# Kernel optimization log

Hardware: AMD Instinct MI355X
Metric: run time of the kernel (lower is better)

Reference implementation:

```python
import jax, jax.numpy as jnp
import numpy as np

N_EMBD = 768
N_HEAD = 12
N_KV_HEAD = 4                      # repeat factor in _repeat_kv
NUM_KV_HEADS = N_HEAD // N_KV_HEAD # 3 actual kv heads
HEAD_DIM = N_EMBD // N_HEAD        # 64
BLOCK_SIZE = 1024                  # sliding window size
SCALE = (HEAD_DIM * N_KV_HEAD / N_HEAD) ** (-0.5)


def _rotary_cos_sin(T, d, dtype):
    inv_freq = 1.0 / (10000.0 ** (jnp.arange(0, d, 2, dtype=jnp.float32) / d))
    t = jnp.arange(T, dtype=jnp.float32)
    freqs = jnp.outer(t, inv_freq)  # (T, d/2)
    return jnp.cos(freqs).astype(dtype)[None, None], jnp.sin(freqs).astype(dtype)[None, None]


def _apply_rotary(x):
    # x: (b, h, T, d)
    T, d = x.shape[2], x.shape[3]
    cos, sin = _rotary_cos_sin(T, d, x.dtype)
    x1, x2 = x[..., : d // 2], x[..., d // 2 :]
    return jnp.concatenate([x1 * cos - x2 * sin, x1 * sin + x2 * cos], axis=-1)


def setup_inputs() -> dict:
    key = jax.random.key(0)
    k0, k1, k2, k3, k4 = jax.random.split(key, 5)
    b, T = 2, 2048
    s = 0.02
    return {
        "hidden_states": jax.random.normal(k0, (b, T, N_EMBD), jnp.float32),
        "Wq": jax.random.normal(k1, (N_HEAD * HEAD_DIM, N_EMBD), jnp.float32) * s,
        "Wk": jax.random.normal(k2, (NUM_KV_HEADS * HEAD_DIM, N_EMBD), jnp.float32) * s,
        "Wv": jax.random.normal(k3, (NUM_KV_HEADS * HEAD_DIM, N_EMBD), jnp.float32) * s,
        "Wo": jax.random.normal(k4, (N_EMBD, N_HEAD * HEAD_DIM), jnp.float32) * s,
    }


def reference(hidden_states, Wq, Wk, Wv, Wo):
    b, T, _ = hidden_states.shape
    q = (hidden_states @ Wq.T).reshape(b, T, N_HEAD, HEAD_DIM).transpose(0, 2, 1, 3)
    k = (hidden_states @ Wk.T).reshape(b, T, NUM_KV_HEADS, HEAD_DIM).transpose(0, 2, 1, 3)
    v = (hidden_states @ Wv.T).reshape(b, T, NUM_KV_HEADS, HEAD_DIM).transpose(0, 2, 1, 3)

    # _repeat_kv: each kv head repeated n_kv_head (=4) times contiguously
    k = jnp.repeat(k, N_KV_HEAD, axis=1)
    v = jnp.repeat(v, N_KV_HEAD, axis=1)

    q = _apply_rotary(q)
    k = _apply_rotary(k)

    # centered sliding-window mask (faithful to per-token loop):
    # window_start = clip(i - W//2, 0, T - W); window is always exactly W wide
    W = BLOCK_SIZE
    i = jnp.arange(T)[:, None]
    j = jnp.arange(T)[None, :]
    start = jnp.clip(i - W // 2, 0, T - W)
    mask = (j >= start) & (j < start + W)  # (T, T)

    scores = jnp.einsum("bhqd,bhkd->bhqk", q, k) * SCALE
    scores = jnp.where(mask[None, None], scores, jnp.finfo(scores.dtype).min)
    attn = jax.nn.softmax(scores, axis=-1)
    out = jnp.einsum("bhqk,bhkd->bhqd", attn, v)  # (b, h, T, d)

    out = out.transpose(0, 2, 1, 3).reshape(b, T, N_EMBD)
    return out @ Wo.T
```

## Files before the change

kernel.cpp:

```cpp
#include <hip/hip_runtime.h>
#include <math.h>

#define T_SEQ 2048
#define E 768
#define WIN 1024
#define KDIM 768
#define HS_SZ ((size_t)4096 * 768)
#define SCALE 0.21650635094610965f

typedef _Float16 f16x8 __attribute__((ext_vector_type(8)));
typedef _Float16 f16x4 __attribute__((ext_vector_type(4)));
typedef float f32x4 __attribute__((ext_vector_type(4)));
typedef __attribute__((address_space(3))) _Float16 lf16;

#define MFMA16(a, b, c) __builtin_amdgcn_mfma_f32_16x16x32_f16(a, b, c, 0, 0, 0)

__device__ __forceinline__ void dma16(const _Float16* g, lf16* l) {
    __builtin_amdgcn_global_load_lds(
        (const __attribute__((address_space(1))) void*)g,
        (__attribute__((address_space(3))) void*)l, 16, 0, 0);
}

__device__ __forceinline__ void cast8(const float* __restrict__ src,
                                      _Float16* __restrict__ dst, int i) {
    float4 a = *(const float4*)&src[i];
    float4 b = *(const float4*)&src[i + 4];
    f16x8 h;
    h[0] = (_Float16)a.x; h[1] = (_Float16)a.y; h[2] = (_Float16)a.z; h[3] = (_Float16)a.w;
    h[4] = (_Float16)b.x; h[5] = (_Float16)b.y; h[6] = (_Float16)b.z; h[7] = (_Float16)b.w;
    *(f16x8*)&dst[i] = h;
}

__global__ __launch_bounds__(256) void prep(
    const float* __restrict__ hs,
    const float* __restrict__ Wq, const float* __restrict__ Wk,
    const float* __restrict__ Wv, const float* __restrict__ Wo,
    _Float16* __restrict__ hs16,
    _Float16* __restrict__ Wq16, _Float16* __restrict__ Wk16,
    _Float16* __restrict__ Wv16, _Float16* __restrict__ Wo16,
    float2* __restrict__ rtab) {
    int tid = blockIdx.x * 256 + threadIdx.x;
    int i = tid * 8;
    if (i < 768 * 768) { cast8(Wq, Wq16, i); cast8(Wo, Wo16, i); }
    if (i < 192 * 768) { cast8(Wk, Wk16, i); cast8(Wv, Wv16, i); }
    cast8(hs, hs16, i);
    if (tid < 2048 * 32) {
        int t = tid >> 5, d = tid & 31;
        float inv = powf(10000.0f, -(float)(2 * d) * (1.0f / 64.0f));
        float s, c;
        sincosf((float)t * inv, &s, &c);
        rtab[tid] = make_float2(c, s);
    }
}

__global__ __launch_bounds__(256) void gemm_qkv(
    const _Float16* __restrict__ A16,
    const _Float16* __restrict__ Wq16, const _Float16* __restrict__ Wk16,
    const _Float16* __restrict__ Wv16, const float2* __restrict__ rtab,
    _Float16* __restrict__ q16, _Float16* __restrict__ k16,
    _Float16* __restrict__ vT16) {
    __shared__ __align__(16) _Float16 As[128 * 128];
    __shared__ __align__(16) _Float16 Bs[64 * 128];
    const int tid = threadIdx.x;
    const int bx = blockIdx.x;
    const int m0 = blockIdx.y * 128;
    const int w = tid >> 6, lane = tid & 63;
    const int mm = lane & 15, quad = lane >> 4;

    const _Float16* bbase; int brb;
    if (bx < 12)      { bbase = Wq16; brb = bx * 64; }
    else if (bx < 15) { bbase = Wk16; brb = (bx - 12) * 64; }
    else              { bbase = Wv16; brb = (bx - 15) * 64; }

    const int rofs4 = lane >> 4;
    const int gs = lane & 15;

    const _Float16* agp[8]; lf16* alp[8];
    #pragma unroll
    for (int j = 0; j < 8; ++j) {
        int c = j * 4 + w;
        int rr = c * 4 + rofs4;
        int glog = gs ^ (rr & 15);
        agp[j] = A16 + (size_t)(m0 + rr) * KDIM + glog * 8;
        alp[j] = ((lf16*)As) + c * 512 + lane * 8;
    }
    const _Float16* bgp[4]; lf16* blp[4];
    #pragma unroll
    for (int j = 0; j < 4; ++j) {
        int c = j * 4 + w;
        int rr = c * 4 + rofs4;
        int glog = gs ^ (rr & 15);
        bgp[j] = bbase + (size_t)(brb + rr) * KDIM + glog * 8;
        blp[j] = ((lf16*)Bs) + c * 512 + lane * 8;
    }

    f32x4 acc[2][4] = {};

    for (int it = 0; it < 6; ++it) {
        const int ke = it * 128;
        __syncthreads();
        #pragma unroll
        for (int j = 0; j < 8; ++j) dma16(agp[j] + ke, alp[j]);
        #pragma unroll
        for (int j = 0; j < 4; ++j) dma16(bgp[j] + ke, blp[j]);
        __syncthreads();
        #pragma unroll
        for (int s = 0; s < 4; ++s) {
            const int gq = ((s * 4 + quad) ^ mm) * 8;
            f16x8 ah[2];
            #pragma unroll
            for (int mt = 0; mt < 2; ++mt)
                ah[mt] = *(const f16x8*)&As[(w * 32 + mt * 16 + mm) * 128 + gq];
            #pragma unroll
            for (int nt = 0; nt < 4; ++nt) {
                f16x8 bh = *(const f16x8*)&Bs[(nt * 16 + mm) * 128 + gq];
                #pragma unroll
                for (int mt = 0; mt < 2; ++mt)
                    acc[mt][nt] = MFMA16(ah[mt], bh, acc[mt][nt]);
            }
        }
    }

    if (bx < 12) {
        #pragma unroll
        for (int mt = 0; mt < 2; ++mt)
            #pragma unroll
            for (int r = 0; r < 4; ++r) {
                int row = m0 + w * 32 + mt * 16 + quad * 4 + r;
                int t = row & (T_SEQ - 1);
                _Float16* dst = &q16[(size_t)row * E + bx * 64 + mm];
                #pragma unroll
                for (int nt = 0; nt < 2; ++nt) {
                    int d = nt * 16 + mm;
                    float2 cs = rtab[t * 32 + d];
                    float x1 = acc[mt][nt][r], x2 = acc[mt][nt + 2][r];
                    dst[nt * 16]       = (_Float16)((x1 * cs.x - x2 * cs.y) * SCALE);
                    dst[(nt + 2) * 16] = (_Float16)((x1 * cs.y + x2 * cs.x) * SCALE);
                }
            }
    } else if (bx < 15) {
        int kvh = bx - 12;
        #pragma unroll
        for (int mt = 0; mt < 2; ++mt)
            #pragma unroll
            for (int r = 0; r < 4; ++r) {
                int row = m0 + w * 32 + mt * 16 + quad * 4 + r;
                int t = row & (T_SEQ - 1);
                int b = row >> 11;
                _Float16* dst = &k16[(((size_t)(b * 3 + kvh)) * T_SEQ + t) * 64 + mm];
                #pragma unroll
                for (int nt = 0; nt < 2; ++nt) {
                    int d = nt * 16 + mm;
                    float2 cs = rtab[t * 32 + d];
                    float x1 = acc[mt][nt][r], x2 = acc[mt][nt + 2][r];
                    dst[nt * 16]       = (_Float16)(x1 * cs.x - x2 * cs.y);
                    dst[(nt + 2) * 16] = (_Float16)(x1 * cs.y + x2 * cs.x);
                }
            }
    } else {
        __syncthreads();
        _Float16 (*vs)[136] = (_Float16 (*)[136])As;
        #pragma unroll
        for (int mt = 0; mt < 2; ++mt)
            #pragma unroll
            for (int nt = 0; nt < 4; ++nt) {
                f16x4 pv;
                #pragma unroll
                for (int r = 0; r < 4; ++r) pv[r] = (_Float16)acc[mt][nt][r];
                *(f16x4*)&vs[nt * 16 + mm][w * 32 + mt * 16 + quad * 4] = pv;
            }
        __syncthreads();
        const int kvh = bx - 15;
        const int b = m0 >> 11, tbase = m0 & (T_SEQ - 1);
        const int tl = (tid & 15) * 8;
        #pragma unroll
        for (int j = 0; j < 4; ++j) {
            int dd = (tid >> 4) + j * 16;
            f16x8 vv = *(const f16x8*)&vs[dd][tl];
            *(f16x8*)&vT16[(((size_t)(b * 3 + kvh)) * 64 + dd) * T_SEQ + tbase + tl] = vv;
        }
    }
}

__global__ __launch_bounds__(256) void gemm_out(
    const _Float16* __restrict__ A16, const _Float16* __restrict__ B16,
    float* __restrict__ C) {
    __shared__ __align__(16) _Float16 As[128 * 128];
    __shared__ __align__(16) _Float16 Bs[64 * 128];
    const int tid = threadIdx.x;
    const int n0 = blockIdx.x * 64;
    const int m0 = blockIdx.y * 128;
    const int w = tid >> 6, lane = tid & 63;
    const int mm = lane & 15, quad = lane >> 4;

    const int rofs4 = lane >> 4;
    const int gs = lane & 15;

    const _Float16* agp[8]; lf16* alp[8];
    #pragma unroll
    for (int j = 0; j < 8; ++j) {
        int c = j * 4 + w;
        int rr = c * 4 + rofs4;
        int glog = gs ^ (rr & 15);
        agp[j] = A16 + (size_t)(m0 + rr) * KDIM + glog * 8;
        alp[j] = ((lf16*)As) + c * 512 + lane * 8;
    }
    const _Float16* bgp[4]; lf16* blp[4];
    #pragma unroll
    for (int j = 0; j < 4; ++j) {
        int c = j * 4 + w;
        int rr = c * 4 + rofs4;
        int glog = gs ^ (rr & 15);
        bgp[j] = B16 + (size_t)(n0 + rr) * KDIM + glog * 8;
        blp[j] = ((lf16*)Bs) + c * 512 + lane * 8;
    }

    f32x4 acc[2][4] = {};

    for (int it = 0; it < 6; ++it) {
        const int ke = it * 128;
        __syncthreads();
        #pragma unroll
        for (int j = 0; j < 8; ++j) dma16(agp[j] + ke, alp[j]);
        #pragma unroll
        for (int j = 0; j < 4; ++j) dma16(bgp[j] + ke, blp[j]);
        __syncthreads();
        #pragma unroll
        for (int s = 0; s < 4; ++s) {
            const int gq = ((s * 4 + quad) ^ mm) * 8;
            f16x8 ah[2];
            #pragma unroll
            for (int mt = 0; mt < 2; ++mt)
                ah[mt] = *(const f16x8*)&As[(w * 32 + mt * 16 + mm) * 128 + gq];
            #pragma unroll
            for (int nt = 0; nt < 4; ++nt) {
                f16x8 bh = *(const f16x8*)&Bs[(nt * 16 + mm) * 128 + gq];
                #pragma unroll
                for (int mt = 0; mt < 2; ++mt)
                    acc[mt][nt] = MFMA16(ah[mt], bh, acc[mt][nt]);
            }
        }
    }

    #pragma unroll
    for (int mt = 0; mt < 2; ++mt)
        #pragma unroll
        for (int r = 0; r < 4; ++r) {
            int row = m0 + w * 32 + mt * 16 + quad * 4 + r;
            float* cp = &C[(size_t)row * 768 + n0 + mm];
            #pragma unroll
            for (int nt = 0; nt < 4; ++nt)
                cp[nt * 16] = acc[mt][nt][r];
        }
}

__global__ __launch_bounds__(256) void attn_mfma(const _Float16* __restrict__ q16,
                                                 const _Float16* __restrict__ k16,
                                                 const _Float16* __restrict__ vT16,
                                                 _Float16* __restrict__ aout16) {
    __shared__ __align__(16) char smem[32768 + 10240];
    _Float16* k_s  = (_Float16*)smem;
    _Float16* vT_s = (_Float16*)(smem + 16384);
    _Float16 (*p_s)[40] = (_Float16(*)[40])(smem + 32768);
    float* ored = (float*)smem;
    float* lred = (float*)(smem + 16384);

    const int b = blockIdx.z, h = blockIdx.y;
    const int i0 = blockIdx.x * 64;
    const int plane = b * 3 + (h >> 2);
    const int tid = threadIdx.x;
    const int w = tid >> 6, lane = tid & 63;
    const int m = lane & 15, quad = lane >> 4;
    const int qh = w & 1, kh = w >> 1;
    const int xm = m & 7;

    int s0 = i0 - 512;      s0 = s0 < 0 ? 0 : (s0 > 1024 ? 1024 : s0);
    int sL = i0 + 63 - 512; sL = sL < 0 ? 0 : (sL > 1024 ? 1024 : sL);
    const int nc = (sL + WIN - s0 + 63) >> 6;

    int start_q[2];
    f16x8 qf[2][2];
    #pragma unroll
    for (int qt = 0; qt < 2; ++qt) {
        int qi = i0 + qh * 32 + qt * 16 + m;
        int sq = qi - 512; sq = sq < 0 ? 0 : (sq > 1024 ? 1024 : sq);
        start_q[qt] = sq;
        const _Float16* qp = &q16[((size_t)(b * T_SEQ + qi)) * E + h * 64 + quad * 8];
        qf[qt][0] = *(const f16x8*)&qp[0];
        qf[qt][1] = *(const f16x8*)&qp[32];
    }

    f32x4 o[2][4] = {};
    float l_run[2] = {0.0f, 0.0f};

    const int rofs = lane >> 3;
    const int glog = (lane & 7) ^ rofs;
    const _Float16* kgb[2]; const _Float16* vgb[2];
    _Float16* klw[2]; _Float16* vlw[2];
    #pragma unroll
    for (int j = 0; j < 2; ++j) {
        int rr = (j * 4 + w) * 8 + rofs;
        kgb[j] = k16 + ((size_t)plane * T_SEQ + rr) * 64 + glog * 8;
        vgb[j] = vT16 + ((size_t)plane * 64 + rr) * T_SEQ + glog * 8;
        klw[j] = k_s + (j * 4 + w) * 512 + lane * 8;
        vlw[j] = vT_s + (j * 4 + w) * 512 + lane * 8;
    }

    f16x8 kr[2], vr[2];
    #pragma unroll
    for (int j = 0; j < 2; ++j) {
        kr[j] = *(const f16x8*)(kgb[j] + (size_t)s0 * 64);
        vr[j] = *(const f16x8*)(vgb[j] + s0);
    }
    #pragma unroll
    for (int j = 0; j < 2; ++j) {
        *(f16x8*)klw[j] = kr[j];
        *(f16x8*)vlw[j] = vr[j];
    }

    for (int ci = 0; ci < nc; ++ci) {
        const int c0 = s0 + ci * 64;
        const int sel = (ci & 1) * 4096;
        __syncthreads();
        if (ci + 1 < nc) {
            const int cn = c0 + 64;
            #pragma unroll
            for (int j = 0; j < 2; ++j) {
                kr[j] = *(const f16x8*)(kgb[j] + (size_t)cn * 64);
                vr[j] = *(const f16x8*)(vgb[j] + cn);
            }
        }

        f32x4 st[2][2] = {};
        #pragma unroll
        for (int s = 0; s < 2; ++s) {
            #pragma unroll
            for (int kt = 0; kt < 2; ++kt) {
                int row = kh * 32 + kt * 16 + m;
                int g = (s * 4 + quad) ^ xm;
                f16x8 a = *(const f16x8*)&k_s[sel + row * 64 + g * 8];
                #pragma unroll
                for (int qt = 0; qt < 2; ++qt)
                    st[kt][qt] = MFMA16(a, qf[qt][s], st[kt][qt]);
            }
        }

        const bool boundary = (c0 < sL) || (c0 + 63 > s0 + 1023);
        if (boundary) {
            #pragma unroll
            for (int kt = 0; kt < 2; ++kt)
                #pragma unroll
                for (int qt = 0; qt < 2; ++qt)
                    #pragma unroll
                    for (int r = 0; r < 4; ++r) {
                        int j = c0 + kh * 32 + kt * 16 + quad * 4 + r;
                        bool valid = (j >= start_q[qt]) && (j < start_q[qt] + WIN);
                        st[kt][qt][r] = valid ? st[kt][qt][r] : -INFINITY;
                    }
        }

        #pragma unroll
        for (int kt = 0; kt < 2; ++kt)
            #pragma unroll
            for (int qt = 0; qt < 2; ++qt) {
                float p0 = __expf(st[kt][qt][0]);
                float p1 = __expf(st[kt][qt][1]);
                float p2 = __expf(st[kt][qt][2]);
                float p3 = __expf(st[kt][qt][3]);
                l_run[qt] += (p0 + p1) + (p2 + p3);
                f16x4 pv = {(_Float16)p0, (_Float16)p1, (_Float16)p2, (_Float16)p3};
                *(f16x4*)&p_s[w * 32 + qt * 16 + m][kt * 16 + quad * 4] = pv;
            }

        f16x8 bp[2];
        #pragma unroll
        for (int qt = 0; qt < 2; ++qt)
            bp[qt] = *(const f16x8*)&p_s[w * 32 + qt * 16 + m][quad * 8];
        #pragma unroll
        for (int mt = 0; mt < 4; ++mt) {
            int g = (kh * 4 + quad) ^ xm;
            f16x8 a = *(const f16x8*)&vT_s[sel + (mt * 16 + m) * 64 + g * 8];
            #pragma unroll
            for (int qt = 0; qt < 2; ++qt)
                o[qt][mt] = MFMA16(a, bp[qt], o[qt][mt]);
        }

        if (ci + 1 < nc) {
            const int ns = ((ci + 1) & 1) * 4096;
            #pragma unroll
            for (int j = 0; j < 2; ++j) {
                *(f16x8*)(klw[j] + ns) = kr[j];
                *(f16x8*)(vlw[j] + ns) = vr[j];
            }
        }
    }

    float l_tot[2];
    #pragma unroll
    for (int qt = 0; qt < 2; ++qt) {
        float l = l_run[qt];
        l += __shfl_xor(l, 16);
        l += __shfl_xor(l, 32);
        l_tot[qt] = l;
    }

    __syncthreads();
    if (kh == 1) {
        #pragma unroll
        for (int qt = 0; qt < 2; ++qt) {
            #pragma unroll
            for (int mt = 0; mt < 4; ++mt) {
                int idx = ((qh * 32 + qt * 16 + m) << 6) + mt * 16 + quad * 4;
                *(float4*)&ored[idx] = *(float4*)&o[qt][mt];
            }
            if (quad == 0) lred[qh * 32 + qt * 16 + m] = l_tot[qt];
        }
    }
    __syncthreads();
    if (kh == 0) {
        #pragma unroll
        for (int qt = 0; qt < 2; ++qt) {
            float rl = 1.0f / (l_tot[qt] + lred[qh * 32 + qt * 16 + m]);
            int qi = i0 + qh * 32 + qt * 16 + m;
            _Float16* op = &aout16[((size_t)(b * T_SEQ + qi)) * E + h * 64];
            #pragma unroll
            for (int mt = 0; mt < 4; ++mt) {
                int idx = ((qh * 32 + qt * 16 + m) << 6) + mt * 16 + quad * 4;
                float4 other = *(float4*)&ored[idx];
                f16x4 hv;
                #pragma unroll
                for (int r = 0; r < 4; ++r)
                    hv[r] = (_Float16)((o[qt][mt][r] + (&other.x)[r]) * rl);
                *(f16x4*)&op[mt * 16 + quad * 4] = hv;
            }
        }
    }
}

extern "C" void kernel_launch(void* const* d_in, const int* in_sizes, int n_in,
                              void* d_out, int out_size, void* d_ws, size_t ws_size,
                              hipStream_t stream) {
    const float* hs = (const float*)d_in[0];
    const float* Wq = (const float*)d_in[1];
    const float* Wk = (const float*)d_in[2];
    const float* Wv = (const float*)d_in[3];
    const float* Wo = (const float*)d_in[4];
    float* out = (float*)d_out;

    _Float16* hs16   = (_Float16*)d_ws;
    _Float16* aout16 = hs16 + HS_SZ;
    _Float16* q16    = aout16 + HS_SZ;
    _Float16* k16    = q16 + HS_SZ;
    _Float16* vT16   = k16 + 6 * 2048 * 64;
    _Float16* Wq16   = vT16 + 6 * 2048 * 64;
    _Float16* Wk16   = Wq16 + 768 * 768;
    _Float16* Wv16   = Wk16 + 192 * 768;
    _Float16* Wo16   = Wv16 + 192 * 768;
    float2*   rtab   = (float2*)(Wo16 + 768 * 768);

    dim3 blk(256);
    prep<<<dim3((int)(HS_SZ / 8 / 256)), blk, 0, stream>>>(hs, Wq, Wk, Wv, Wo,
                                                           hs16, Wq16, Wk16, Wv16, Wo16, rtab);
    gemm_qkv<<<dim3(18, 32), blk, 0, stream>>>(hs16, Wq16, Wk16, Wv16, rtab, q16, k16, vT16);
    attn_mfma<<<dim3(32, 12, 2), blk, 0, stream>>>(q16, k16, vT16, aout16);
    gemm_out<<<dim3(12, 32), blk, 0, stream>>>(aout16, Wo16, out);
}
```

Measured before the change: 133.2 us.

## Fuse all four stages into one persistent kernel with grid barriers

Replaces the four separate launches (cast prep, QKV GEMM, attention, output GEMM) with one persistent kernel of 512 blocks. The stages are separated by software grid-wide barriers built on atomics, and each stage walks its jobs in a grid-stride loop. The aim is to remove launch gaps between the kernels. In exchange it adds a memset launch, three spin barriers, and limits occupancy to two blocks per CU with a 48KB shared buffer. The barriers deadlock if all 512 blocks are not resident at once, and some blocks take two jobs in the QKV and attention stages, which creates load imbalance.

```diff
diff --git a/kernel.cpp b/kernel.cpp
--- a/kernel.cpp
+++ b/kernel.cpp
@@ -7,6 +7,7 @@
 #define KDIM 768
 #define HS_SZ ((size_t)4096 * 768)
 #define SCALE 0.21650635094610965f
+#define NBLK 512u
 
 typedef _Float16 f16x8 __attribute__((ext_vector_type(8)));
 typedef _Float16 f16x4 __attribute__((ext_vector_type(4)));
@@ -31,409 +32,415 @@
     *(f16x8*)&dst[i] = h;
 }
 
-__global__ __launch_bounds__(256) void prep(
+__device__ __forceinline__ void gbar(unsigned* c) {
+    __syncthreads();
+    if (threadIdx.x == 0) {
+        __threadfence();
+        __hip_atomic_fetch_add(c, 1u, __ATOMIC_ACQ_REL, __HIP_MEMORY_SCOPE_AGENT);
+        while (__hip_atomic_load(c, __ATOMIC_ACQUIRE, __HIP_MEMORY_SCOPE_AGENT) < NBLK)
+            __builtin_amdgcn_s_sleep(2);
+        __threadfence();
+    }
+    __syncthreads();
+}
+
+__global__ __launch_bounds__(256, 2) void fused(
     const float* __restrict__ hs,
     const float* __restrict__ Wq, const float* __restrict__ Wk,
     const float* __restrict__ Wv, const float* __restrict__ Wo,
-    _Float16* __restrict__ hs16,
+    float* __restrict__ out,
+    _Float16* __restrict__ hs16, _Float16* __restrict__ aout16,
+    _Float16* __restrict__ q16, _Float16* __restrict__ k16,
+    _Float16* __restrict__ vT16,
     _Float16* __restrict__ Wq16, _Float16* __restrict__ Wk16,
     _Float16* __restrict__ Wv16, _Float16* __restrict__ Wo16,
-    float2* __restrict__ rtab) {
-    int tid = blockIdx.x * 256 + threadIdx.x;
-    int i = tid * 8;
-    if (i < 768 * 768) { cast8(Wq, Wq16, i); cast8(Wo, Wo16, i); }
-    if (i < 192 * 768) { cast8(Wk, Wk16, i); cast8(Wv, Wv16, i); }
-    cast8(hs, hs16, i);
-    if (tid < 2048 * 32) {
-        int t = tid >> 5, d = tid & 31;
-        float inv = powf(10000.0f, -(float)(2 * d) * (1.0f / 64.0f));
-        float s, c;
-        sincosf((float)t * inv, &s, &c);
-        rtab[tid] = make_float2(c, s);
-    }
-}
-
-__global__ __launch_bounds__(256) void gemm_qkv(
-    const _Float16* __restrict__ A16,
-    const _Float16* __restrict__ Wq16, const _Float16* __restrict__ Wk16,
-    const _Float16* __restrict__ Wv16, const float2* __restrict__ rtab,
-    _Float16* __restrict__ q16, _Float16* __restrict__ k16,
-    _Float16* __restrict__ vT16) {
-    __shared__ __align__(16) _Float16 As[128 * 128];
-    __shared__ __align__(16) _Float16 Bs[64 * 128];
+    float2* __restrict__ rtab, unsigned* __restrict__ bar) {
+    __shared__ __align__(16) char smem[49152];
+    const int bid = blockIdx.x;
     const int tid = threadIdx.x;
-    const int bx = blockIdx.x;
-    const int m0 = blockIdx.y * 128;
     const int w = tid >> 6, lane = tid & 63;
     const int mm = lane & 15, quad = lane >> 4;
 
-    const _Float16* bbase; int brb;
-    if (bx < 12)      { bbase = Wq16; brb = bx * 64; }
-    else if (bx < 15) { bbase = Wk16; brb = (bx - 12) * 64; }
-    else              { bbase = Wv16; brb = (bx - 15) * 64; }
-
-    const int rofs4 = lane >> 4;
-    const int gs = lane & 15;
-
-    const _Float16* agp[8]; lf16* alp[8];
-    #pragma unroll
-    for (int j = 0; j < 8; ++j) {
-        int c = j * 4 + w;
-        int rr = c * 4 + rofs4;
-        int glog = gs ^ (rr & 15);
-        agp[j] = A16 + (size_t)(m0 + rr) * KDIM + glog * 8;
-        alp[j] = ((lf16*)As) + c * 512 + lane * 8;
+    for (int g = bid * 256 + tid; g < 393216; g += 131072) {
+        int i = g * 8;
+        cast8(hs, hs16, i);
+        if (i < 768 * 768) { cast8(Wq, Wq16, i); cast8(Wo, Wo16, i); }
+        if (i < 192 * 768) { cast8(Wk, Wk16, i); cast8(Wv, Wv16, i); }
+        if (g < 2048 * 32) {
+            int t = g >> 5, d = g & 31;
+            float inv = powf(10000.0f, -(float)(2 * d) * (1.0f / 64.0f));
+            float s, c;
+            sincosf((float)t * inv, &s, &c);
+            rtab[g] = make_float2(c, s);
+        }
     }
-    const _Float16* bgp[4]; lf16* blp[4];
-    #pragma unroll
-    for (int j = 0; j < 4; ++j) {
-        int c = j * 4 + w;
-        int rr = c * 4 + rofs4;
-        int glog = gs ^ (rr & 15);
-        bgp[j] = bbase + (size_t)(brb + rr) * KDIM + glog * 8;
-        blp[j] = ((lf16*)Bs) + c * 512 + lane * 8;
+    gbar(&bar[0]);
+
+    for (int job = bid; job < 576; job += NBLK) {
+        _Float16* As = (_Float16*)smem;
+        _Float16* Bs = (_Float16*)(smem + 32768);
+        const int bx = job % 18;
+        const int m0 = (job / 18) * 128;
+
+        const _Float16* bbase; int brb;
+        if (bx < 12)      { bbase = Wq16; brb = bx * 64; }
+        else if (bx < 15) { bbase = Wk16; brb = (bx - 12) * 64; }
+        else              { bbase = Wv16; brb = (bx - 15) * 64; }
+
+        const int rofs4 = lane >> 4;
+        const int gs = lane & 15;
+
+        const _Float16* agp[8]; lf16* alp[8];
+        #pragma unroll
+        for (int j = 0; j < 8; ++j) {
+            int c = j * 4 + w;
+            int rr = c * 4 + rofs4;
+            int glog = gs ^ (rr & 15);
+            agp[j] = hs16 + (size_t)(m0 + rr) * KDIM + glog * 8;
+            alp[j] = ((lf16*)As) + c * 512 + lane * 8;
+        }
+        const _Float16* bgp[4]; lf16* blp[4];
+        #pragma unroll
+        for (int j = 0; j < 4; ++j) {
+            int c = j * 4 + w;
+            int rr = c * 4 + rofs4;
+            int glog = gs ^ (rr & 15);
+            bgp[j] = bbase + (size_t)(brb + rr) * KDIM + glog * 8;
+            blp[j] = ((lf16*)Bs) + c * 512 + lane * 8;
+        }
+
+        f32x4 acc[2][4] = {};
+
+        for (int it = 0; it < 6; ++it) {
+            const int ke = it * 128;
+            __syncthreads();
+            #pragma unroll
+            for (int j = 0; j < 8; ++j) dma16(agp[j] + ke, alp[j]);
+            #pragma unroll
+            for (int j = 0; j < 4; ++j) dma16(bgp[j] + ke, blp[j]);
+            __syncthreads();
+            #pragma unroll
+            for (int s = 0; s < 4; ++s) {
+                const int gq = ((s * 4 + quad) ^ mm) * 8;
+                f16x8 ah[2];
+                #pragma unroll
+                for (int mt = 0; mt < 2; ++mt)
+                    ah[mt] = *(const f16x8*)&As[(w * 32 + mt * 16 + mm) * 128 + gq];
+                #pragma unroll
+                for (int nt = 0; nt < 4; ++nt) {
+                    f16x8 bh = *(const f16x8*)&Bs[(nt * 16 + mm) * 128 + gq];
+                    #pragma unroll
+                    for (int mt = 0; mt < 2; ++mt)
+                        acc[mt][nt] = MFMA16(ah[mt], bh, acc[mt][nt]);
+                }
+            }
+        }
+
+        if (bx < 12) {
+            #pragma unroll
+            for (int mt = 0; mt < 2; ++mt)
+                #pragma unroll
+                for (int r = 0; r < 4; ++r) {
+                    int row = m0 + w * 32 + mt * 16 + quad * 4 + r;
+                    int t = row & (T_SEQ - 1);
+                    _Float16* dst = &q16[(size_t)row * E + bx * 64 + mm];
+                    #pragma unroll
+                    for (int nt = 0; nt < 2; ++nt) {
+                        int d = nt * 16 + mm;
+                        float2 cs = rtab[t * 32 + d];
+                        float x1 = acc[mt][nt][r], x2 = acc[mt][nt + 2][r];
+                        dst[nt * 16]       = (_Float16)((x1 * cs.x - x2 * cs.y) * SCALE);
+                        dst[(nt + 2) * 16] = (_Float16)((x1 * cs.y + x2 * cs.x) * SCALE);
+                    }
+                }
+        } else if (bx < 15) {
+            int kvh = bx - 12;
+            #pragma unroll
+            for (int mt = 0; mt < 2; ++mt)
+                #pragma unroll
+                for (int r = 0; r < 4; ++r) {
+                    int row = m0 + w * 32 + mt * 16 + quad * 4 + r;
+                    int t = row & (T_SEQ - 1);
+                    int b = row >> 11;
+                    _Float16* dst = &k16[(((size_t)(b * 3 + kvh)) * T_SEQ + t) * 64 + mm];
+                    #pragma unroll
+                    for (int nt = 0; nt < 2; ++nt) {
+                        int d = nt * 16 + mm;
+                        float2 cs = rtab[t * 32 + d];
+                        float x1 = acc[mt][nt][r], x2 = acc[mt][nt + 2][r];
+                        dst[nt * 16]       = (_Float16)(x1 * cs.x - x2 * cs.y);
+                        dst[(nt + 2) * 16] = (_Float16)(x1 * cs.y + x2 * cs.x);
+                    }
+                }
+        } else {
+            __syncthreads();
+            _Float16 (*vs)[136] = (_Float16 (*)[136])As;
+            #pragma unroll
+            for (int mt = 0; mt < 2; ++mt)
+                #pragma unroll
+                for (int nt = 0; nt < 4; ++nt) {
+                    f16x4 pv;
+                    #pragma unroll
+                    for (int r = 0; r < 4; ++r) pv[r] = (_Float16)acc[mt][nt][r];
+                    *(f16x4*)&vs[nt * 16 + mm][w * 32 + mt * 16 + quad * 4] = pv;
+                }
+            __syncthreads();
+            const int kvh = bx - 15;
+            const int b = m0 >> 11, tbase = m0 & (T_SEQ - 1);
+            const int tl = (tid & 15) * 8;
+            #pragma unroll
+            for (int j = 0; j < 4; ++j) {
+                int dd = (tid >> 4) + j * 16;
+                f16x8 vv = *(const f16x8*)&vs[dd][tl];
+                *(f16x8*)&vT16[(((size_t)(b * 3 + kvh)) * 64 + dd) * T_SEQ + tbase + tl] = vv;
+            }
+        }
     }
-
-    f32x4 acc[2][4] = {};
-
-    for (int it = 0; it < 6; ++it) {
-        const int ke = it * 128;
+    gbar(&bar[1]);
+
+    for (int job = bid; job < 768; job += NBLK) {
         __syncthreads();
-        #pragma unroll
-        for (int j = 0; j < 8; ++j) dma16(agp[j] + ke, alp[j]);
-        #pragma unroll
-        for (int j = 0; j < 4; ++j) dma16(bgp[j] + ke, blp[j]);
+        _Float16* k_s  = (_Float16*)smem;
+        _Float16* vT_s = (_Float16*)(smem + 16384);
+        _Float16 (*p_s)[40] = (_Float16(*)[40])(smem + 32768);
+        float* ored = (float*)smem;
+        float* lred = (float*)(smem + 16384);
+
+        const int b = job / 384;
+        const int h = (job >> 5) % 12;
+        const int i0 = (job & 31) * 64;
+        const int plane = b * 3 + (h >> 2);
+        const int qh = w & 1, kh = w >> 1;
+        const int xm = mm & 7;
+
+        int s0 = i0 - 512;      s0 = s0 < 0 ? 0 : (s0 > 1024 ? 1024 : s0);
+        int sL = i0 + 63 - 512; sL = sL < 0 ? 0 : (sL > 1024 ? 1024 : sL);
+        const int nc = (sL + WIN - s0 + 63) >> 6;
+
+        int start_q[2];
+        f16x8 qf[2][2];
+        #pragma unroll
+        for (int qt = 0; qt < 2; ++qt) {
+            int qi = i0 + qh * 32 + qt * 16 + mm;
+            int sq = qi - 512; sq = sq < 0 ? 0 : (sq > 1024 ? 1024 : sq);
+            start_q[qt] = sq;
+            const _Float16* qp = &q16[((size_t)(b * T_SEQ + qi)) * E + h * 64 + quad * 8];
+            qf[qt][0] = *(const f16x8*)&qp[0];
+            qf[qt][1] = *(const f16x8*)&qp[32];
+        }
+
+        f32x4 o[2][4] = {};
+        float l_run[2] = {0.0f, 0.0f};
+
+        const int rofs = lane >> 3;
+        const int glog = (lane & 7) ^ rofs;
+        const _Float16* kgb[2]; const _Float16* vgb[2];
+        _Float16* klw[2]; _Float16* vlw[2];
+        #pragma unroll
+        for (int j = 0; j < 2; ++j) {
+            int rr = (j * 4 + w) * 8 + rofs;
+            kgb[j] = k16 + ((size_t)plane * T_SEQ + rr) * 64 + glog * 8;
+            vgb[j] = vT16 + ((size_t)plane * 64 + rr) * T_SEQ + glog * 8;
+            klw[j] = k_s + (j * 4 + w) * 512 + lane * 8;
+            vlw[j] = vT_s + (j * 4 + w) * 512 + lane * 8;
+        }
+
+        f16x8 kr[2], vr[2];
+        #pragma unroll
+        for (int j = 0; j < 2; ++j) {
+            kr[j] = *(const f16x8*)(kgb[j] + (size_t)s0 * 64);
+            vr[j] = *(const f16x8*)(vgb[j] + s0);
+        }
+        #pragma unroll
+        for (int j = 0; j < 2; ++j) {
+            *(f16x8*)klw[j] = kr[j];
+            *(f16x8*)vlw[j] = vr[j];
+        }
+
+        for (int ci = 0; ci < nc; ++ci) {
+            const int c0 = s0 + ci * 64;
+            const int sel = (ci & 1) * 4096;
+            __syncthreads();
+            if (ci + 1 < nc) {
+                const int cn = c0 + 64;
+                #pragma unroll
+                for (int j = 0; j < 2; ++j) {
+                    kr[j] = *(const f16x8*)(kgb[j] + (size_t)cn * 64);
+                    vr[j] = *(const f16x8*)(vgb[j] + cn);
+                }
+            }
+
+            f32x4 st[2][2] = {};
+            #pragma unroll
+            for (int s = 0; s < 2; ++s) {
+                #pragma unroll
+                for (int kt = 0; kt < 2; ++kt) {
+                    int row = kh * 32 + kt * 16 + mm;
+                    int g = (s * 4 + quad) ^ xm;
+                    f16x8 a = *(const f16x8*)&k_s[sel + row * 64 + g * 8];
+                    #pragma unroll
+                    for (int qt = 0; qt < 2; ++qt)
+                        st[kt][qt] = MFMA16(a, qf[qt][s], st[kt][qt]);
+                }
+            }
+
+            const bool boundary = (c0 < sL) || (c0 + 63 > s0 + 1023);
+            if (boundary) {
+                #pragma unroll
+                for (int kt = 0; kt < 2; ++kt)
+                    #pragma unroll
+                    for (int qt = 0; qt < 2; ++qt)
+                        #pragma unroll
+                        for (int r = 0; r < 4; ++r) {
+                            int j = c0 + kh * 32 + kt * 16 + quad * 4 + r;
+                            bool valid = (j >= start_q[qt]) && (j < start_q[qt] + WIN);
+                            st[kt][qt][r] = valid ? st[kt][qt][r] : -INFINITY;
+                        }
+            }
+
+            #pragma unroll
+            for (int kt = 0; kt < 2; ++kt)
+                #pragma unroll
+                for (int qt = 0; qt < 2; ++qt) {
+                    float p0 = __expf(st[kt][qt][0]);
+                    float p1 = __expf(st[kt][qt][1]);
+                    float p2 = __expf(st[kt][qt][2]);
+                    float p3 = __expf(st[kt][qt][3]);
+                    l_run[qt] += (p0 + p1) + (p2 + p3);
+                    f16x4 pv = {(_Float16)p0, (_Float16)p1, (_Float16)p2, (_Float16)p3};
+                    *(f16x4*)&p_s[w * 32 + qt * 16 + mm][kt * 16 + quad * 4] = pv;
+                }
+
+            f16x8 bp[2];
+            #pragma unroll
+            for (int qt = 0; qt < 2; ++qt)
+                bp[qt] = *(const f16x8*)&p_s[w * 32 + qt * 16 + mm][quad * 8];
+            #pragma unroll
+            for (int mt = 0; mt < 4; ++mt) {
+                int g = (kh * 4 + quad) ^ xm;
+                f16x8 a = *(const f16x8*)&vT_s[sel + (mt * 16 + mm) * 64 + g * 8];
+                #pragma unroll
+                for (int qt = 0; qt < 2; ++qt)
+                    o[qt][mt] = MFMA16(a, bp[qt], o[qt][mt]);
+            }
+
+            if (ci + 1 < nc) {
+                const int ns = ((ci + 1) & 1) * 4096;
+                #pragma unroll
+                for (int j = 0; j < 2; ++j) {
+                    *(f16x8*)(klw[j] + ns) = kr[j];
+                    *(f16x8*)(vlw[j] + ns) = vr[j];
+                }
+            }
+        }
+
+        float l_tot[2];
+        #pragma unroll
+        for (int qt = 0; qt < 2; ++qt) {
+            float l = l_run[qt];
+            l += __shfl_xor(l, 16);
+            l += __shfl_xor(l, 32);
+            l_tot[qt] = l;
+        }
+
         __syncthreads();
-        #pragma unroll
-        for (int s = 0; s < 4; ++s) {
-            const int gq = ((s * 4 + quad) ^ mm) * 8;
-            f16x8 ah[2];
-            #pragma unroll
-            for (int mt = 0; mt < 2; ++mt)
-                ah[mt] = *(const f16x8*)&As[(w * 32 + mt * 16 + mm) * 128 + gq];
-            #pragma unroll
-            for (int nt = 0; nt < 4; ++nt) {
-                f16x8 bh = *(const f16x8*)&Bs[(nt * 16 + mm) * 128 + gq];
+        if (kh == 1) {
+            #pragma unroll
+            for (int qt = 0; qt < 2; ++qt) {
+                #pragma unroll
+                for (int mt = 0; mt < 4; ++mt) {
+                    int idx = ((qh * 32 + qt * 16 + mm) << 6) + mt * 16 + quad * 4;
+                    *(float4*)&ored[idx] = *(float4*)&o[qt][mt];
+                }
+                if (quad == 0) lred[qh * 32 + qt * 16 + mm] = l_tot[qt];
+            }
+        }
+        __syncthreads();
+        if (kh == 0) {
+            #pragma unroll
+            for (int qt = 0; qt < 2; ++qt) {
+                float rl = 1.0f / (l_tot[qt] + lred[qh * 32 + qt * 16 + mm]);
+                int qi = i0 + qh * 32 + qt * 16 + mm;
+                _Float16* op = &aout16[((size_t)(b * T_SEQ + qi)) * E + h * 64];
+                #pragma unroll
+                for (int mt = 0; mt < 4; ++mt) {
+                    int idx = ((qh * 32 + qt * 16 + mm) << 6) + mt * 16 + quad * 4;
+                    float4 other = *(float4*)&ored[idx];
+                    f16x4 hv;
+                    #pragma unroll
+                    for (int r = 0; r < 4; ++r)
+                        hv[r] = (_Float16)((o[qt][mt][r] + (&other.x)[r]) * rl);
+                    *(f16x4*)&op[mt * 16 + quad * 4] = hv;
+                }
+            }
+        }
+    }
+    gbar(&bar[2]);
+
+    if (bid < 384) {
+        _Float16* As = (_Float16*)smem;
+        _Float16* Bs = (_Float16*)(smem + 32768);
+        const int n0 = (bid % 12) * 64;
+        const int m0 = (bid / 12) * 128;
+
+        const int rofs4 = lane >> 4;
+        const int gs = lane & 15;
+
+        const _Float16* agp[8]; lf16* alp[8];
+        #pragma unroll
+        for (int j = 0; j < 8; ++j) {
+            int c = j * 4 + w;
+            int rr = c * 4 + rofs4;
+            int glog = gs ^ (rr & 15);
+            agp[j] = aout16 + (size_t)(m0 + rr) * KDIM + glog * 8;
+            alp[j] = ((lf16*)As) + c * 512 + lane * 8;
+        }
+        const _Float16* bgp[4]; lf16* blp[4];
+        #pragma unroll
+        for (int j = 0; j < 4; ++j) {
+            int c = j * 4 + w;
+            int rr = c * 4 + rofs4;
+            int glog = gs ^ (rr & 15);
+            bgp[j] = Wo16 + (size_t)(n0 + rr) * KDIM + glog * 8;
+            blp[j] = ((lf16*)Bs) + c * 512 + lane * 8;
+        }
+
+        f32x4 acc[2][4] = {};
+
+        for (int it = 0; it < 6; ++it) {
+            const int ke = it * 128;
+            __syncthreads();
+            #pragma unroll
+            for (int j = 0; j < 8; ++j) dma16(agp[j] + ke, alp[j]);
+            #pragma unroll
+            for (int j = 0; j < 4; ++j) dma16(bgp[j] + ke, blp[j]);
+            __syncthreads();
+            #pragma unroll
+            for (int s = 0; s < 4; ++s) {
+                const int gq = ((s * 4 + quad) ^ mm) * 8;
+                f16x8 ah[2];
                 #pragma unroll
                 for (int mt = 0; mt < 2; ++mt)
-                    acc[mt][nt] = MFMA16(ah[mt], bh, acc[mt][nt]);
-            }
-        }
-    }
-
-    if (bx < 12) {
+                    ah[mt] = *(const f16x8*)&As[(w * 32 + mt * 16 + mm) * 128 + gq];
+                #pragma unroll
+                for (int nt = 0; nt < 4; ++nt) {
+                    f16x8 bh = *(const f16x8*)&Bs[(nt * 16 + mm) * 128 + gq];
+                    #pragma unroll
+                    for (int mt = 0; mt < 2; ++mt)
+                        acc[mt][nt] = MFMA16(ah[mt], bh, acc[mt][nt]);
+                }
+            }
+        }
         #pragma unroll
         for (int mt = 0; mt < 2; ++mt)
             #pragma unroll
             for (int r = 0; r < 4; ++r) {
                 int row = m0 + w * 32 + mt * 16 + quad * 4 + r;
-                int t = row & (T_SEQ - 1);
-                _Float16* dst = &q16[(size_t)row * E + bx * 64 + mm];
-                #pragma unroll
-                for (int nt = 0; nt < 2; ++nt) {
-                    int d = nt * 16 + mm;
-                    float2 cs = rtab[t * 32 + d];
-                    float x1 = acc[mt][nt][r], x2 = acc[mt][nt + 2][r];
-                    dst[nt * 16]       = (_Float16)((x1 * cs.x - x2 * cs.y) * SCALE);
-                    dst[(nt + 2) * 16] = (_Float16)((x1 * cs.y + x2 * cs.x) * SCALE);
-                }
-            }
-    } else if (bx < 15) {
-        int kvh = bx - 12;
-        #pragma unroll
-        for (int mt = 0; mt < 2; ++mt)
-            #pragma unroll
-            for (int r = 0; r < 4; ++r) {
-                int row = m0 + w * 32 + mt * 16 + quad * 4 + r;
-                int t = row & (T_SEQ - 1);
-                int b = row >> 11;
-                _Float16* dst = &k16[(((size_t)(b * 3 + kvh)) * T_SEQ + t) * 64 + mm];
-                #pragma unroll
-                for (int nt = 0; nt < 2; ++nt) {
-                    int d = nt * 16 + mm;
-                    float2 cs = rtab[t * 32 + d];
-                    float x1 = acc[mt][nt][r], x2 = acc[mt][nt + 2][r];
-                    dst[nt * 16]       = (_Float16)(x1 * cs.x - x2 * cs.y);
-                    dst[(nt + 2) * 16] = (_Float16)(x1 * cs.y + x2 * cs.x);
-                }
-            }
-    } else {
-        __syncthreads();
-        _Float16 (*vs)[136] = (_Float16 (*)[136])As;
-        #pragma unroll
-        for (int mt = 0; mt < 2; ++mt)
-            #pragma unroll
-            for (int nt = 0; nt < 4; ++nt) {
-                f16x4 pv;
-                #pragma unroll
-                for (int r = 0; r < 4; ++r) pv[r] = (_Float16)acc[mt][nt][r];
-                *(f16x4*)&vs[nt * 16 + mm][w * 32 + mt * 16 + quad * 4] = pv;
-            }
-        __syncthreads();
-        const int kvh = bx - 15;
-        const int b = m0 >> 11, tbase = m0 & (T_SEQ - 1);
-        const int tl = (tid & 15) * 8;
-        #pragma unroll
-        for (int j = 0; j < 4; ++j) {
-            int dd = (tid >> 4) + j * 16;
-            f16x8 vv = *(const f16x8*)&vs[dd][tl];
-            *(f16x8*)&vT16[(((size_t)(b * 3 + kvh)) * 64 + dd) * T_SEQ + tbase + tl] = vv;
-        }
-    }
-}
-
-__global__ __launch_bounds__(256) void gemm_out(
-    const _Float16* __restrict__ A16, const _Float16* __restrict__ B16,
-    float* __restrict__ C) {
-    __shared__ __align__(16) _Float16 As[128 * 128];
-    __shared__ __align__(16) _Float16 Bs[64 * 128];
-    const int tid = threadIdx.x;
-    const int n0 = blockIdx.x * 64;
-    const int m0 = blockIdx.y * 128;
-    const int w = tid >> 6, lane = tid & 63;
-    const int mm = lane & 15, quad = lane >> 4;
-
-    const int rofs4 = lane >> 4;
-    const int gs = lane & 15;
-
-    const _Float16* agp[8]; lf16* alp[8];
-    #pragma unroll
-    for (int j = 0; j < 8; ++j) {
-        int c = j * 4 + w;
-        int rr = c * 4 + rofs4;
-        int glog = gs ^ (rr & 15);
-        agp[j] = A16 + (size_t)(m0 + rr) * KDIM + glog * 8;
-        alp[j] = ((lf16*)As) + c * 512 + lane * 8;
-    }
-    const _Float16* bgp[4]; lf16* blp[4];
-    #pragma unroll
-    for (int j = 0; j < 4; ++j) {
-        int c = j * 4 + w;
-        int rr = c * 4 + rofs4;
-        int glog = gs ^ (rr & 15);
-        bgp[j] = B16 + (size_t)(n0 + rr) * KDIM + glog * 8;
-        blp[j] = ((lf16*)Bs) + c * 512 + lane * 8;
-    }
-
-    f32x4 acc[2][4] = {};
-
-    for (int it = 0; it < 6; ++it) {
-        const int ke = it * 128;
-        __syncthreads();
-        #pragma unroll
-        for (int j = 0; j < 8; ++j) dma16(agp[j] + ke, alp[j]);
-        #pragma unroll
-        for (int j = 0; j < 4; ++j) dma16(bgp[j] + ke, blp[j]);
-        __syncthreads();
-        #pragma unroll
-        for (int s = 0; s < 4; ++s) {
-            const int gq = ((s * 4 + quad) ^ mm) * 8;
-            f16x8 ah[2];
-            #pragma unroll
-            for (int mt = 0; mt < 2; ++mt)
-                ah[mt] = *(const f16x8*)&As[(w * 32 + mt * 16 + mm) * 128 + gq];
-            #pragma unroll
-            for (int nt = 0; nt < 4; ++nt) {
-                f16x8 bh = *(const f16x8*)&Bs[(nt * 16 + mm) * 128 + gq];
-                #pragma unroll
-                for (int mt = 0; mt < 2; ++mt)
-                    acc[mt][nt] = MFMA16(ah[mt], bh, acc[mt][nt]);
-            }
-        }
-    }
-
-    #pragma unroll
-    for (int mt = 0; mt < 2; ++mt)
-        #pragma unroll
-        for (int r = 0; r < 4; ++r) {
-            int row = m0 + w * 32 + mt * 16 + quad * 4 + r;
-            float* cp = &C[(size_t)row * 768 + n0 + mm];
-            #pragma unroll
-            for (int nt = 0; nt < 4; ++nt)
-                cp[nt * 16] = acc[mt][nt][r];
-        }
-}
-
-__global__ __launch_bounds__(256) void attn_mfma(const _Float16* __restrict__ q16,
-                                                 const _Float16* __restrict__ k16,
-                                                 const _Float16* __restrict__ vT16,
-                                                 _Float16* __restrict__ aout16) {
-    __shared__ __align__(16) char smem[32768 + 10240];
-    _Float16* k_s  = (_Float16*)smem;
-    _Float16* vT_s = (_Float16*)(smem + 16384);
-    _Float16 (*p_s)[40] = (_Float16(*)[40])(smem + 32768);
-    float* ored = (float*)smem;
-    float* lred = (float*)(smem + 16384);
-
-    const int b = blockIdx.z, h = blockIdx.y;
-    const int i0 = blockIdx.x * 64;
-    const int plane = b * 3 + (h >> 2);
-    const int tid = threadIdx.x;
-    const int w = tid >> 6, lane = tid & 63;
-    const int m = lane & 15, quad = lane >> 4;
-    const int qh = w & 1, kh = w >> 1;
-    const int xm = m & 7;
-
-    int s0 = i0 - 512;      s0 = s0 < 0 ? 0 : (s0 > 1024 ? 1024 : s0);
-    int sL = i0 + 63 - 512; sL = sL < 0 ? 0 : (sL > 1024 ? 1024 : sL);
-    const int nc = (sL + WIN - s0 + 63) >> 6;
-
-    int start_q[2];
-    f16x8 qf[2][2];
-    #pragma unroll
-    for (int qt = 0; qt < 2; ++qt) {
-        int qi = i0 + qh * 32 + qt * 16 + m;
-        int sq = qi - 512; sq = sq < 0 ? 0 : (sq > 1024 ? 1024 : sq);
-        start_q[qt] = sq;
-        const _Float16* qp = &q16[((size_t)(b * T_SEQ + qi)) * E + h * 64 + quad * 8];
-        qf[qt][0] = *(const f16x8*)&qp[0];
-        qf[qt][1] = *(const f16x8*)&qp[32];
-    }
-
-    f32x4 o[2][4] = {};
-    float l_run[2] = {0.0f, 0.0f};
-
-    const int rofs = lane >> 3;
-    const int glog = (lane & 7) ^ rofs;
-    const _Float16* kgb[2]; const _Float16* vgb[2];
-    _Float16* klw[2]; _Float16* vlw[2];
-    #pragma unroll
-    for (int j = 0; j < 2; ++j) {
-        int rr = (j * 4 + w) * 8 + rofs;
-        kgb[j] = k16 + ((size_t)plane * T_SEQ + rr) * 64 + glog * 8;
-        vgb[j] = vT16 + ((size_t)plane * 64 + rr) * T_SEQ + glog * 8;
-        klw[j] = k_s + (j * 4 + w) * 512 + lane * 8;
-        vlw[j] = vT_s + (j * 4 + w) * 512 + lane * 8;
-    }
-
-    f16x8 kr[2], vr[2];
-    #pragma unroll
-    for (int j = 0; j < 2; ++j) {
-        kr[j] = *(const f16x8*)(kgb[j] + (size_t)s0 * 64);
-        vr[j] = *(const f16x8*)(vgb[j] + s0);
-    }
-    #pragma unroll
-    for (int j = 0; j < 2; ++j) {
-        *(f16x8*)klw[j] = kr[j];
-        *(f16x8*)vlw[j] = vr[j];
-    }
-
-    for (int ci = 0; ci < nc; ++ci) {
-        const int c0 = s0 + ci * 64;
-        const int sel = (ci & 1) * 4096;
-        __syncthreads();
-        if (ci + 1 < nc) {
-            const int cn = c0 + 64;
-            #pragma unroll
-            for (int j = 0; j < 2; ++j) {
-                kr[j] = *(const f16x8*)(kgb[j] + (size_t)cn * 64);
-                vr[j] = *(const f16x8*)(vgb[j] + cn);
-            }
-        }
-
-        f32x4 st[2][2] = {};
-        #pragma unroll
-        for (int s = 0; s < 2; ++s) {
-            #pragma unroll
-            for (int kt = 0; kt < 2; ++kt) {
-                int row = kh * 32 + kt * 16 + m;
-                int g = (s * 4 + quad) ^ xm;
-                f16x8 a = *(const f16x8*)&k_s[sel + row * 64 + g * 8];
-                #pragma unroll
-                for (int qt = 0; qt < 2; ++qt)
-                    st[kt][qt] = MFMA16(a, qf[qt][s], st[kt][qt]);
-            }
-        }
-
-        const bool boundary = (c0 < sL) || (c0 + 63 > s0 + 1023);
-        if (boundary) {
-            #pragma unroll
-            for (int kt = 0; kt < 2; ++kt)
-                #pragma unroll
-                for (int qt = 0; qt < 2; ++qt)
-                    #pragma unroll
-                    for (int r = 0; r < 4; ++r) {
-                        int j = c0 + kh * 32 + kt * 16 + quad * 4 + r;
-                        bool valid = (j >= start_q[qt]) && (j < start_q[qt] + WIN);
-                        st[kt][qt][r] = valid ? st[kt][qt][r] : -INFINITY;
-                    }
-        }
-
-        #pragma unroll
-        for (int kt = 0; kt < 2; ++kt)
-            #pragma unroll
-            for (int qt = 0; qt < 2; ++qt) {
-                float p0 = __expf(st[kt][qt][0]);
-                float p1 = __expf(st[kt][qt][1]);
-                float p2 = __expf(st[kt][qt][2]);
-                float p3 = __expf(st[kt][qt][3]);
-                l_run[qt] += (p0 + p1) + (p2 + p3);
-                f16x4 pv = {(_Float16)p0, (_Float16)p1, (_Float16)p2, (_Float16)p3};
-                *(f16x4*)&p_s[w * 32 + qt * 16 + m][kt * 16 + quad * 4] = pv;
-            }
-
-        f16x8 bp[2];
-        #pragma unroll
-        for (int qt = 0; qt < 2; ++qt)
-            bp[qt] = *(const f16x8*)&p_s[w * 32 + qt * 16 + m][quad * 8];
-        #pragma unroll
-        for (int mt = 0; mt < 4; ++mt) {
-            int g = (kh * 4 + quad) ^ xm;
-            f16x8 a = *(const f16x8*)&vT_s[sel + (mt * 16 + m) * 64 + g * 8];
-            #pragma unroll
-            for (int qt = 0; qt < 2; ++qt)
-                o[qt][mt] = MFMA16(a, bp[qt], o[qt][mt]);
-        }
-
-        if (ci + 1 < nc) {
-            const int ns = ((ci + 1) & 1) * 4096;
-            #pragma unroll
-            for (int j = 0; j < 2; ++j) {
-                *(f16x8*)(klw[j] + ns) = kr[j];
-                *(f16x8*)(vlw[j] + ns) = vr[j];
-            }
-        }
-    }
-
-    float l_tot[2];
-    #pragma unroll
-    for (int qt = 0; qt < 2; ++qt) {
-        float l = l_run[qt];
-        l += __shfl_xor(l, 16);
-        l += __shfl_xor(l, 32);
-        l_tot[qt] = l;
-    }
-
-    __syncthreads();
-    if (kh == 1) {
-        #pragma unroll
-        for (int qt = 0; qt < 2; ++qt) {
-            #pragma unroll
-            for (int mt = 0; mt < 4; ++mt) {
-                int idx = ((qh * 32 + qt * 16 + m) << 6) + mt * 16 + quad * 4;
-                *(float4*)&ored[idx] = *(float4*)&o[qt][mt];
-            }
-            if (quad == 0) lred[qh * 32 + qt * 16 + m] = l_tot[qt];
-        }
-    }
-    __syncthreads();
-    if (kh == 0) {
-        #pragma unroll
-        for (int qt = 0; qt < 2; ++qt) {
-            float rl = 1.0f / (l_tot[qt] + lred[qh * 32 + qt * 16 + m]);
-            int qi = i0 + qh * 32 + qt * 16 + m;
-            _Float16* op = &aout16[((size_t)(b * T_SEQ + qi)) * E + h * 64];
-            #pragma unroll
-            for (int mt = 0; mt < 4; ++mt) {
-                int idx = ((qh * 32 + qt * 16 + m) << 6) + mt * 16 + quad * 4;
-                float4 other = *(float4*)&ored[idx];
-                f16x4 hv;
-                #pragma unroll
-                for (int r = 0; r < 4; ++r)
-                    hv[r] = (_Float16)((o[qt][mt][r] + (&other.x)[r]) * rl);
-                *(f16x4*)&op[mt * 16 + quad * 4] = hv;
-            }
-        }
+                float* cp = &out[(size_t)row * 768 + n0 + mm];
+                #pragma unroll
+                for (int nt = 0; nt < 4; ++nt)
+                    cp[nt * 16] = acc[mt][nt][r];
+            }
     }
 }
 
@@ -457,11 +464,10 @@
     _Float16* Wv16   = Wk16 + 192 * 768;
     _Float16* Wo16   = Wv16 + 192 * 768;
     float2*   rtab   = (float2*)(Wo16 + 768 * 768);
-
-    dim3 blk(256);
-    prep<<<dim3((int)(HS_SZ / 8 / 256)), blk, 0, stream>>>(hs, Wq, Wk, Wv, Wo,
-                                                           hs16, Wq16, Wk16, Wv16, Wo16, rtab);
-    gemm_qkv<<<dim3(18, 32), blk, 0, stream>>>(hs16, Wq16, Wk16, Wv16, rtab, q16, k16, vT16);
-    attn_mfma<<<dim3(32, 12, 2), blk, 0, stream>>>(q16, k16, vT16, aout16);
-    gemm_out<<<dim3(12, 32), blk, 0, stream>>>(aout16, Wo16, out);
+    unsigned* bar    = (unsigned*)(rtab + 2048 * 32);
+
+    hipMemsetAsync(bar, 0, 64, stream);
+    fused<<<dim3(NBLK), dim3(256), 0, stream>>>(
+        hs, Wq, Wk, Wv, Wo, out, hs16, aout16, q16, k16, vT16,
+        Wq16, Wk16, Wv16, Wo16, rtab, bar);
 }
```

Measured after the change: 441.5 us. +231.5%, slower.
